# Performance work log

Hardware: AMD Instinct MI355X
Metric: run time of the kernel (lower is better)

Reference implementation:

```python
import jax, jax.numpy as jnp
import numpy as np

B, S, F = 64, 512, 128
H = 512            # LSTM hidden (conv_channels entries)
D0, D1 = 512, 256  # dense_sizes
P, FPP = 24, 4     # predictions, features_per_prediction


def _lstm_layer(x, Wx, Wh, b):
    """Flax OptimizedLSTMCell math: gates i,f,g,o; input matmul has no bias,
    hidden matmul carries the bias; carry initialized to zeros."""
    Bc, Sc, _ = x.shape
    Hc = Wh.shape[0]
    # Precompute input contribution for all timesteps: [B, S, 4H]
    xg = jnp.einsum('bsd,dg->bsg', x, Wx)

    def step(carry, xg_t):
        c, h = carry
        g = xg_t + h @ Wh + b            # [B, 4H]
        i, f, gg, o = jnp.split(g, 4, axis=-1)
        c = jax.nn.sigmoid(f) * c + jax.nn.sigmoid(i) * jnp.tanh(gg)
        h = jax.nn.sigmoid(o) * jnp.tanh(c)
        return (c, h), h

    init = (jnp.zeros((Bc, Hc), x.dtype), jnp.zeros((Bc, Hc), x.dtype))
    _, hs = jax.lax.scan(step, init, jnp.swapaxes(xg, 0, 1))  # [S, B, H]
    return jnp.swapaxes(hs, 0, 1)


def setup_inputs() -> dict:
    key = jax.random.key(0)
    ks = jax.random.split(key, 12)
    g = lambda k, shape, fan_in: jax.random.normal(k, shape, jnp.float32) / np.sqrt(fan_in)
    return {
        'x':    jax.random.normal(ks[0], (B, S, F), jnp.float32),
        'Wx0':  g(ks[1], (F, 4 * H), F),
        'Wh0':  g(ks[2], (H, 4 * H), H),
        'b0':   jnp.zeros((4 * H,), jnp.float32),
        'Wx1':  g(ks[3], (H, 4 * H), H),
        'Wh1':  g(ks[4], (H, 4 * H), H),
        'b1':   jnp.zeros((4 * H,), jnp.float32),
        'Wd0':  g(ks[5], (H, D0), H),
        'bd0':  jnp.zeros((D0,), jnp.float32),
        'Wd1':  g(ks[6], (D0, D1), D0),
        'bd1':  jnp.zeros((D1,), jnp.float32),
        'Wout': g(ks[7], (D1, P * FPP), D1),
        'bout': jnp.zeros((P * FPP,), jnp.float32),
        'train': 0,
    }


def reference(x, Wx0, Wh0, b0, Wx1, Wh1, b1, Wd0, bd0, Wd1, bd1, Wout, bout, train):
    # down_scale == 1 -> no max_pool; dropout == 0 -> no dropout.
    h = _lstm_layer(x, Wx0, Wh0, b0)   # [B, S, H]
    h = _lstm_layer(h, Wx1, Wh1, b1)   # [B, S, H]
    h = h[:, -1, :]                    # last timestep [B, H]
    h = jax.nn.relu(h @ Wd0 + bd0)
    h = jax.nn.relu(h @ Wd1 + bd1)
    out = h @ Wout + bout              # [B, P*FPP]
    out = out.reshape((-1, P, FPP))
    return jax.nn.sigmoid(out)
```

## Files before the change

### kernel.cpp

```cpp
#include <hip/hip_runtime.h>

typedef __attribute__((ext_vector_type(8))) short short8;
typedef __attribute__((ext_vector_type(4))) float f32x4;

#define NB 64
#define NS 512
#define NF 128
#define NH 512
#define NG 2048
#define NBLK 256

__device__ __forceinline__ unsigned short f2bf(float f) {
    unsigned int u = __builtin_bit_cast(unsigned int, f);
    u = (u + 0x7fffu + ((u >> 16) & 1u)) >> 16;
    return (unsigned short)u;
}
__device__ __forceinline__ float sigm(float x) { return 1.0f / (1.0f + __expf(-x)); }
__device__ __forceinline__ float tanh_(float x) {
    float e = __expf(2.0f * fabsf(x));
    float r = 1.0f - 2.0f / (e + 1.0f);
    return x < 0.0f ? -r : r;
}

__device__ __forceinline__ short8 cohld16(const unsigned short* p) {
    unsigned long long* q = (unsigned long long*)p;
    union { unsigned long long u[2]; short8 s; } v;
    v.u[0] = __hip_atomic_load(q,     __ATOMIC_RELAXED, __HIP_MEMORY_SCOPE_AGENT);
    v.u[1] = __hip_atomic_load(q + 1, __ATOMIC_RELAXED, __HIP_MEMORY_SCOPE_AGENT);
    return v.s;
}
__device__ __forceinline__ void cohst2(unsigned short* p, unsigned short v) {
    __hip_atomic_store(p, v, __ATOMIC_RELAXED, __HIP_MEMORY_SCOPE_AGENT);
}

__device__ __forceinline__ void flag_wait(const unsigned* flags, int lane, unsigned tgt) {
    while (__hip_atomic_load(&flags[lane], __ATOMIC_RELAXED, __HIP_MEMORY_SCOPE_AGENT) < tgt)
        __builtin_amdgcn_s_sleep(1);
    __builtin_amdgcn_sched_barrier(0);
    asm volatile("" ::: "memory");
}
__device__ __forceinline__ void flag_signal(unsigned* myflag, unsigned val, int lane) {
    asm volatile("s_waitcnt vmcnt(0)" ::: "memory");
    if (lane == 0)
        __hip_atomic_store(myflag, val, __ATOMIC_RELAXED, __HIP_MEMORY_SCOPE_AGENT);
}

__global__ void cvt_bf16(const float* __restrict__ in, unsigned short* __restrict__ out, int n) {
    int i = blockIdx.x * blockDim.x + threadIdx.x;
    int stride = gridDim.x * blockDim.x;
    for (; i < n; i += stride) out[i] = f2bf(in[i]);
}

__global__ void tr_cvt(const float* __restrict__ in, unsigned short* __restrict__ out, int K, int N) {
    int i = blockIdx.x * blockDim.x + threadIdx.x;
    if (i >= K * N) return;
    int n = i / K, k = i - n * K;
    out[i] = f2bf(in[k * N + n]);
}

__global__ void __launch_bounds__(64, 1) lstm_coop(
    const unsigned short* __restrict__ xbf,
    unsigned short* __restrict__ h0,
    unsigned short* __restrict__ h1,
    const unsigned short* __restrict__ whT0,
    const unsigned short* __restrict__ wxT0,
    const unsigned short* __restrict__ whT1,
    const unsigned short* __restrict__ wxT1,
    const float* __restrict__ b0,
    const float* __restrict__ b1,
    float* __restrict__ hlast,
    unsigned* __restrict__ flagbase)
{
    __shared__ unsigned short w0lds[32 * 640];
    __shared__ unsigned short w1lds[32 * 1024];

    const int lane = threadIdx.x;
    const int c16  = lane & 15;
    const int kg   = lane >> 4;
    const int bg   = blockIdx.x >> 6;
    const int ct   = blockIdx.x & 63;
    unsigned* flagA = (unsigned*)((char*)flagbase + (size_t)bg * 4096);
    unsigned* flagB = (unsigned*)((char*)flagbase + (size_t)bg * 4096 + 2048);

    auto loadw = [&](unsigned short* dst, const unsigned short* whT,
                     const unsigned short* wxT, int Kx, int rowB) {
        int cpr = (NH + Kx) >> 3;
        for (int idx = lane; idx < 32 * cpr; idx += 64) {
            int n = idx / cpr, cc = idx - n * cpr;
            int G = (n >> 3) * NH + ct * 8 + (n & 7);
            uint4 v = (cc < 64) ? *(const uint4*)(whT + (size_t)G * NH + cc * 8)
                                : *(const uint4*)(wxT + (size_t)G * Kx + (size_t)(cc - 64) * 8);
            *(uint4*)((char*)dst + n * rowB + ((cc * 16) ^ ((n & 7) << 4))) = v;
        }
    };
    loadw(w0lds, whT0, wxT0, NF, 1280);
    loadw(w1lds, whT1, wxT1, NH, 2048);
    __syncthreads();

    const int hc8 = c16 & 7;
    const float bi0 = b0[0 * NH + ct * 8 + hc8], bf0 = b0[1 * NH + ct * 8 + hc8];
    const float bg0 = b0[2 * NH + ct * 8 + hc8], bo0 = b0[3 * NH + ct * 8 + hc8];
    const float bi1 = b1[0 * NH + ct * 8 + hc8], bf1 = b1[1 * NH + ct * 8 + hc8];
    const float bg1 = b1[2 * NH + ct * 8 + hc8], bo1 = b1[3 * NH + ct * 8 + hc8];

    const int arow = bg * 16 + c16;
    const size_t aseq = (size_t)arow * NS;
    float cst0[4] = {0.f, 0.f, 0.f, 0.f};
    float cst1[4] = {0.f, 0.f, 0.f, 0.f};

    const char* lA0 = (const char*)w0lds + (size_t)c16 * 1280;
    const char* lB0 = (const char*)w0lds + (size_t)(16 + c16) * 1280;
    const char* lA1 = (const char*)w1lds + (size_t)c16 * 2048;
    const char* lB1 = (const char*)w1lds + (size_t)(16 + c16) * 2048;
    const int swz = (c16 & 7) << 4;

    auto epilogue = [&](f32x4 acc0, f32x4 acc1, float* cst,
                        float bi, float bf_, float bgt, float bo,
                        unsigned short* hseq, int t, bool wlast) {
        f32x4 s0, s1;
        #pragma unroll
        for (int i = 0; i < 4; ++i) {
            s0[i] = __shfl_xor(acc0[i], 8, 64);
            s1[i] = __shfl_xor(acc1[i], 8, 64);
        }
        const bool lower = (c16 < 8);
        unsigned short* hw = hseq + ((size_t)(bg * 16 + kg * 4) * NS + t) * NH + ct * 8 + hc8;
        #pragma unroll
        for (int i = 0; i < 4; ++i) {
            float gi = (lower ? acc0[i] : s0[i]) + bi;
            float gf = (lower ? s0[i] : acc0[i]) + bf_;
            float gg = (lower ? acc1[i] : s1[i]) + bgt;
            float go = (lower ? s1[i] : acc1[i]) + bo;
            float c_ = sigm(gf) * cst[i] + sigm(gi) * tanh_(gg);
            cst[i] = c_;
            float hv = sigm(go) * tanh_(c_);
            if (lower) {
                cohst2(hw + (size_t)i * NS * NH, f2bf(hv));
                if (wlast)
                    hlast[(bg * 16 + kg * 4 + i) * NH + ct * 8 + hc8] = hv;
            }
        }
    };

    short8 hfrag[16];

    for (int r = 0; r <= NS; ++r) {
        if (r > 0) {
            flag_wait(flagA, lane, (unsigned)r);
            const unsigned short* hp = h0 + (aseq + (r - 1)) * NH + kg * 8;
            #pragma unroll
            for (int ks = 0; ks < 16; ++ks) hfrag[ks] = cohld16(hp + ks * 32);
        }
        if (r < NS) {
            f32x4 a0 = {0.f, 0.f, 0.f, 0.f};
            f32x4 a1 = {0.f, 0.f, 0.f, 0.f};
            const unsigned short* xp = xbf + (aseq + r) * NF + kg * 8;
            #pragma unroll
            for (int ks = 0; ks < 4; ++ks) {
                short8 a = *(const short8*)(xp + ks * 32);
                int boff = 1024 + ks * 64 + kg * 16;
                a0 = __builtin_amdgcn_mfma_f32_16x16x32_bf16(a, *(const short8*)(lA0 + (boff ^ swz)), a0, 0, 0, 0);
                a1 = __builtin_amdgcn_mfma_f32_16x16x32_bf16(a, *(const short8*)(lB0 + (boff ^ swz)), a1, 0, 0, 0);
            }
            if (r > 0) {
                #pragma unroll
                for (int ks = 0; ks < 16; ++ks) {
                    int boff = ks * 64 + kg * 16;
                    a0 = __builtin_amdgcn_mfma_f32_16x16x32_bf16(hfrag[ks], *(const short8*)(lA0 + (boff ^ swz)), a0, 0, 0, 0);
                    a1 = __builtin_amdgcn_mfma_f32_16x16x32_bf16(hfrag[ks], *(const short8*)(lB0 + (boff ^ swz)), a1, 0, 0, 0);
                }
            }
            epilogue(a0, a1, cst0, bi0, bf0, bg0, bo0, h0, r, false);
            flag_signal(&flagA[ct], (unsigned)(r + 1), lane);
        }
        if (r > 0) {
            int t1 = r - 1;
            flag_wait(flagB, lane, (unsigned)t1);
            f32x4 a0 = {0.f, 0.f, 0.f, 0.f};
            f32x4 a1 = {0.f, 0.f, 0.f, 0.f};
            #pragma unroll
            for (int ks = 0; ks < 16; ++ks) {
                int boff = 1024 + ks * 64 + kg * 16;
                a0 = __builtin_amdgcn_mfma_f32_16x16x32_bf16(hfrag[ks], *(const short8*)(lA1 + (boff ^ swz)), a0, 0, 0, 0);
                a1 = __builtin_amdgcn_mfma_f32_16x16x32_bf16(hfrag[ks], *(const short8*)(lB1 + (boff ^ swz)), a1, 0, 0, 0);
            }
            if (t1 > 0) {
                const unsigned short* hp = h1 + (aseq + (t1 - 1)) * NH + kg * 8;
                #pragma unroll
                for (int ks = 0; ks < 16; ++ks) {
                    short8 a = cohld16(hp + ks * 32);
                    int boff = ks * 64 + kg * 16;
                    a0 = __builtin_amdgcn_mfma_f32_16x16x32_bf16(a, *(const short8*)(lA1 + (boff ^ swz)), a0, 0, 0, 0);
                    a1 = __builtin_amdgcn_mfma_f32_16x16x32_bf16(a, *(const short8*)(lB1 + (boff ^ swz)), a1, 0, 0, 0);
                }
            }
            epilogue(a0, a1, cst1, bi1, bf1, bg1, bo1, h1, t1, t1 == NS - 1);
            flag_signal(&flagB[ct], (unsigned)(t1 + 1), lane);
        }
    }
}

__global__ void dense(const float* __restrict__ in, const float* __restrict__ W,
                      const float* __restrict__ bias, float* __restrict__ out,
                      int K, int N, int mode) {
    int b = blockIdx.x;
    int j = threadIdx.x;
    extern __shared__ float srow[];
    for (int k = j; k < K; k += blockDim.x) srow[k] = in[b * K + k];
    __syncthreads();
    if (j < N) {
        float acc = bias[j];
        for (int k = 0; k < K; ++k) acc += srow[k] * W[k * N + j];
        if (mode == 1) acc = fmaxf(acc, 0.0f);
        else           acc = 1.0f / (1.0f + __expf(-acc));
        out[b * N + j] = acc;
    }
}

extern "C" void kernel_launch(void* const* d_in, const int* in_sizes, int n_in,
                              void* d_out, int out_size, void* d_ws, size_t ws_size,
                              hipStream_t stream) {
    const float* x    = (const float*)d_in[0];
    const float* Wx0  = (const float*)d_in[1];
    const float* Wh0  = (const float*)d_in[2];
    const float* b0   = (const float*)d_in[3];
    const float* Wx1  = (const float*)d_in[4];
    const float* Wh1  = (const float*)d_in[5];
    const float* b1   = (const float*)d_in[6];
    const float* Wd0  = (const float*)d_in[7];
    const float* bd0  = (const float*)d_in[8];
    const float* Wd1  = (const float*)d_in[9];
    const float* bd1  = (const float*)d_in[10];
    const float* Wout = (const float*)d_in[11];
    const float* bout = (const float*)d_in[12];

    char* ws = (char*)d_ws;
    size_t off = 0;
    auto alloc = [&](size_t bytes) { void* p = ws + off; off += (bytes + 255) & ~255ull; return p; };
    unsigned* flagbase = (unsigned*)alloc(4 * 4096);
    unsigned short* xbf  = (unsigned short*)alloc((size_t)NB * NS * NF * 2);
    unsigned short* h0   = (unsigned short*)alloc((size_t)NB * NS * NH * 2);
    unsigned short* h1   = (unsigned short*)alloc((size_t)NB * NS * NH * 2);
    unsigned short* whT0 = (unsigned short*)alloc((size_t)NG * NH * 2);
    unsigned short* wxT0 = (unsigned short*)alloc((size_t)NG * NF * 2);
    unsigned short* whT1 = (unsigned short*)alloc((size_t)NG * NH * 2);
    unsigned short* wxT1 = (unsigned short*)alloc((size_t)NG * NH * 2);
    float* hlast = (float*)alloc((size_t)NB * NH * 4);
    float* dt0   = (float*)alloc((size_t)NB * 512 * 4);
    float* dt1   = (float*)alloc((size_t)NB * 256 * 4);

    hipMemsetAsync(flagbase, 0, 4 * 4096, stream);
    cvt_bf16<<<2048, 256, 0, stream>>>(x, xbf, NB * NS * NF);
    tr_cvt<<<(NG * NF + 255) / 256, 256, 0, stream>>>(Wx0, wxT0, NF, NG);
    tr_cvt<<<(NG * NH + 255) / 256, 256, 0, stream>>>(Wh0, whT0, NH, NG);
    tr_cvt<<<(NG * NH + 255) / 256, 256, 0, stream>>>(Wx1, wxT1, NH, NG);
    tr_cvt<<<(NG * NH + 255) / 256, 256, 0, stream>>>(Wh1, whT1, NH, NG);

    void* args[] = { (void*)&xbf, (void*)&h0, (void*)&h1,
                     (void*)&whT0, (void*)&wxT0, (void*)&whT1, (void*)&wxT1,
                     (void*)&b0, (void*)&b1, (void*)&hlast, (void*)&flagbase };
    hipLaunchCooperativeKernel((void*)lstm_coop, dim3(NBLK), dim3(64), args, 0, stream);

    dense<<<NB, 512, 512 * 4, stream>>>(hlast, Wd0, bd0, dt0, 512, 512, 1);
    dense<<<NB, 256, 512 * 4, stream>>>(dt0, Wd1, bd1, dt1, 512, 256, 1);
    dense<<<NB, 128, 256 * 4, stream>>>(dt1, Wout, bout, (float*)d_out, 256, 96, 2);
}
```

Before: 4.658 ms.

## Replace flag barriers with tagged double-buffered hidden-state slots polled directly

Drops the per-step flag arrays and stores each hidden value as a 32-bit word that carries a timestep tag in its upper half. Consumers poll the data itself until every tag matches, so the separate flag write, wait and reload round trip goes away. The full h sequences are replaced by two-slot ring buffers, and the layer-0 input matmul now runs before the poll so it overlaps the wait. The cost is twice the bytes per hidden value and a heavier polling loop. Ring-buffer correctness relies on producers never running more than one step ahead of consumers.

```diff
diff --git a/kernel.cpp b/kernel.cpp
--- a/kernel.cpp
+++ b/kernel.cpp
@@ -9,6 +9,7 @@
 #define NH 512
 #define NG 2048
 #define NBLK 256
+#define TH_SLOT (64 * 512)
 
 __device__ __forceinline__ unsigned short f2bf(float f) {
     unsigned int u = __builtin_bit_cast(unsigned int, f);
@@ -22,29 +23,6 @@
     return x < 0.0f ? -r : r;
 }
 
-__device__ __forceinline__ short8 cohld16(const unsigned short* p) {
-    unsigned long long* q = (unsigned long long*)p;
-    union { unsigned long long u[2]; short8 s; } v;
-    v.u[0] = __hip_atomic_load(q,     __ATOMIC_RELAXED, __HIP_MEMORY_SCOPE_AGENT);
-    v.u[1] = __hip_atomic_load(q + 1, __ATOMIC_RELAXED, __HIP_MEMORY_SCOPE_AGENT);
-    return v.s;
-}
-__device__ __forceinline__ void cohst2(unsigned short* p, unsigned short v) {
-    __hip_atomic_store(p, v, __ATOMIC_RELAXED, __HIP_MEMORY_SCOPE_AGENT);
-}
-
-__device__ __forceinline__ void flag_wait(const unsigned* flags, int lane, unsigned tgt) {
-    while (__hip_atomic_load(&flags[lane], __ATOMIC_RELAXED, __HIP_MEMORY_SCOPE_AGENT) < tgt)
-        __builtin_amdgcn_s_sleep(1);
-    __builtin_amdgcn_sched_barrier(0);
-    asm volatile("" ::: "memory");
-}
-__device__ __forceinline__ void flag_signal(unsigned* myflag, unsigned val, int lane) {
-    asm volatile("s_waitcnt vmcnt(0)" ::: "memory");
-    if (lane == 0)
-        __hip_atomic_store(myflag, val, __ATOMIC_RELAXED, __HIP_MEMORY_SCOPE_AGENT);
-}
-
 __global__ void cvt_bf16(const float* __restrict__ in, unsigned short* __restrict__ out, int n) {
     int i = blockIdx.x * blockDim.x + threadIdx.x;
     int stride = gridDim.x * blockDim.x;
@@ -60,16 +38,15 @@
 
 __global__ void __launch_bounds__(64, 1) lstm_coop(
     const unsigned short* __restrict__ xbf,
-    unsigned short* __restrict__ h0,
-    unsigned short* __restrict__ h1,
+    unsigned* __restrict__ th0,
+    unsigned* __restrict__ th1,
     const unsigned short* __restrict__ whT0,
     const unsigned short* __restrict__ wxT0,
     const unsigned short* __restrict__ whT1,
     const unsigned short* __restrict__ wxT1,
     const float* __restrict__ b0,
     const float* __restrict__ b1,
-    float* __restrict__ hlast,
-    unsigned* __restrict__ flagbase)
+    float* __restrict__ hlast)
 {
     __shared__ unsigned short w0lds[32 * 640];
     __shared__ unsigned short w1lds[32 * 1024];
@@ -79,8 +56,6 @@
     const int kg   = lane >> 4;
     const int bg   = blockIdx.x >> 6;
     const int ct   = blockIdx.x & 63;
-    unsigned* flagA = (unsigned*)((char*)flagbase + (size_t)bg * 4096);
-    unsigned* flagB = (unsigned*)((char*)flagbase + (size_t)bg * 4096 + 2048);
 
     auto loadw = [&](unsigned short* dst, const unsigned short* whT,
                      const unsigned short* wxT, int Kx, int rowB) {
@@ -114,9 +89,60 @@
     const char* lB1 = (const char*)w1lds + (size_t)(16 + c16) * 2048;
     const int swz = (c16 & 7) << 4;
 
+    auto poll_tensor = [&](const unsigned* tslot, unsigned want, short8* frag) {
+        const unsigned long long* p0 =
+            (const unsigned long long*)(tslot + (size_t)arow * NH) + kg * 4;
+        for (int b = 0; b < 2; ++b) {
+            for (;;) {
+                unsigned bad = 0;
+                #pragma unroll
+                for (int j = 0; j < 8; ++j) {
+                    unsigned w0 = __hip_atomic_load(
+                        (const unsigned*)(p0 + (size_t)(b * 8 + j) * 16),
+                        __ATOMIC_RELAXED, __HIP_MEMORY_SCOPE_AGENT);
+                    bad |= (w0 >> 16) ^ want;
+                }
+                if (__ballot(bad != 0) == 0ull) break;
+            }
+            for (;;) {
+                unsigned long long d[8][4];
+                #pragma unroll
+                for (int j = 0; j < 8; ++j)
+                    #pragma unroll
+                    for (int w = 0; w < 4; ++w)
+                        d[j][w] = __hip_atomic_load(
+                            p0 + (size_t)(b * 8 + j) * 16 + w,
+                            __ATOMIC_RELAXED, __HIP_MEMORY_SCOPE_AGENT);
+                unsigned bad = 0;
+                #pragma unroll
+                for (int j = 0; j < 8; ++j)
+                    #pragma unroll
+                    for (int w = 0; w < 4; ++w) {
+                        unsigned long long x = d[j][w];
+                        bad |= (((unsigned)(x >> 16) & 0xFFFFu) ^ want)
+                             | ((unsigned)(x >> 48) ^ want);
+                    }
+                if (__ballot(bad != 0) == 0ull) {
+                    #pragma unroll
+                    for (int j = 0; j < 8; ++j) {
+                        short8 s;
+                        #pragma unroll
+                        for (int w = 0; w < 4; ++w) {
+                            s[2 * w]     = (short)(unsigned short)(d[j][w] & 0xFFFFu);
+                            s[2 * w + 1] = (short)(unsigned short)((d[j][w] >> 32) & 0xFFFFu);
+                        }
+                        frag[b * 8 + j] = s;
+                    }
+                    break;
+                }
+            }
+        }
+        __builtin_amdgcn_sched_barrier(0);
+    };
+
     auto epilogue = [&](f32x4 acc0, f32x4 acc1, float* cst,
                         float bi, float bf_, float bgt, float bo,
-                        unsigned short* hseq, int t, bool wlast) {
+                        unsigned* tslot, unsigned tag, bool wlast) {
         f32x4 s0, s1;
         #pragma unroll
         for (int i = 0; i < 4; ++i) {
@@ -124,7 +150,7 @@
             s1[i] = __shfl_xor(acc1[i], 8, 64);
         }
         const bool lower = (c16 < 8);
-        unsigned short* hw = hseq + ((size_t)(bg * 16 + kg * 4) * NS + t) * NH + ct * 8 + hc8;
+        unsigned* tw = tslot + (size_t)(bg * 16 + kg * 4) * NH + ct * 8 + hc8;
         #pragma unroll
         for (int i = 0; i < 4; ++i) {
             float gi = (lower ? acc0[i] : s0[i]) + bi;
@@ -135,7 +161,9 @@
             cst[i] = c_;
             float hv = sigm(go) * tanh_(c_);
             if (lower) {
-                cohst2(hw + (size_t)i * NS * NH, f2bf(hv));
+                __hip_atomic_store(tw + (size_t)i * NH,
+                                   (tag << 16) | (unsigned)f2bf(hv),
+                                   __ATOMIC_RELAXED, __HIP_MEMORY_SCOPE_AGENT);
                 if (wlast)
                     hlast[(bg * 16 + kg * 4 + i) * NH + ct * 8 + hc8] = hv;
             }
@@ -145,15 +173,9 @@
     short8 hfrag[16];
 
     for (int r = 0; r <= NS; ++r) {
-        if (r > 0) {
-            flag_wait(flagA, lane, (unsigned)r);
-            const unsigned short* hp = h0 + (aseq + (r - 1)) * NH + kg * 8;
-            #pragma unroll
-            for (int ks = 0; ks < 16; ++ks) hfrag[ks] = cohld16(hp + ks * 32);
-        }
+        f32x4 a0 = {0.f, 0.f, 0.f, 0.f};
+        f32x4 a1 = {0.f, 0.f, 0.f, 0.f};
         if (r < NS) {
-            f32x4 a0 = {0.f, 0.f, 0.f, 0.f};
-            f32x4 a1 = {0.f, 0.f, 0.f, 0.f};
             const unsigned short* xp = xbf + (aseq + r) * NF + kg * 8;
             #pragma unroll
             for (int ks = 0; ks < 4; ++ks) {
@@ -162,6 +184,9 @@
                 a0 = __builtin_amdgcn_mfma_f32_16x16x32_bf16(a, *(const short8*)(lA0 + (boff ^ swz)), a0, 0, 0, 0);
                 a1 = __builtin_amdgcn_mfma_f32_16x16x32_bf16(a, *(const short8*)(lB0 + (boff ^ swz)), a1, 0, 0, 0);
             }
+        }
+        if (r > 0) poll_tensor(th0 + ((r - 1) & 1) * TH_SLOT, (unsigned)r, hfrag);
+        if (r < NS) {
             if (r > 0) {
                 #pragma unroll
                 for (int ks = 0; ks < 16; ++ks) {
@@ -170,32 +195,30 @@
                     a1 = __builtin_amdgcn_mfma_f32_16x16x32_bf16(hfrag[ks], *(const short8*)(lB0 + (boff ^ swz)), a1, 0, 0, 0);
                 }
             }
-            epilogue(a0, a1, cst0, bi0, bf0, bg0, bo0, h0, r, false);
-            flag_signal(&flagA[ct], (unsigned)(r + 1), lane);
+            epilogue(a0, a1, cst0, bi0, bf0, bg0, bo0,
+                     th0 + (r & 1) * TH_SLOT, (unsigned)(r + 1), false);
         }
         if (r > 0) {
             int t1 = r - 1;
-            flag_wait(flagB, lane, (unsigned)t1);
-            f32x4 a0 = {0.f, 0.f, 0.f, 0.f};
-            f32x4 a1 = {0.f, 0.f, 0.f, 0.f};
+            f32x4 c0 = {0.f, 0.f, 0.f, 0.f};
+            f32x4 c1 = {0.f, 0.f, 0.f, 0.f};
             #pragma unroll
             for (int ks = 0; ks < 16; ++ks) {
                 int boff = 1024 + ks * 64 + kg * 16;
-                a0 = __builtin_amdgcn_mfma_f32_16x16x32_bf16(hfrag[ks], *(const short8*)(lA1 + (boff ^ swz)), a0, 0, 0, 0);
-                a1 = __builtin_amdgcn_mfma_f32_16x16x32_bf16(hfrag[ks], *(const short8*)(lB1 + (boff ^ swz)), a1, 0, 0, 0);
+                c0 = __builtin_amdgcn_mfma_f32_16x16x32_bf16(hfrag[ks], *(const short8*)(lA1 + (boff ^ swz)), c0, 0, 0, 0);
+                c1 = __builtin_amdgcn_mfma_f32_16x16x32_bf16(hfrag[ks], *(const short8*)(lB1 + (boff ^ swz)), c1, 0, 0, 0);
             }
             if (t1 > 0) {
-                const unsigned short* hp = h1 + (aseq + (t1 - 1)) * NH + kg * 8;
+                poll_tensor(th1 + (r & 1) * TH_SLOT, (unsigned)t1, hfrag);
                 #pragma unroll
                 for (int ks = 0; ks < 16; ++ks) {
-                    short8 a = cohld16(hp + ks * 32);
                     int boff = ks * 64 + kg * 16;
-                    a0 = __builtin_amdgcn_mfma_f32_16x16x32_bf16(a, *(const short8*)(lA1 + (boff ^ swz)), a0, 0, 0, 0);
-                    a1 = __builtin_amdgcn_mfma_f32_16x16x32_bf16(a, *(const short8*)(lB1 + (boff ^ swz)), a1, 0, 0, 0);
-                }
-            }
-            epilogue(a0, a1, cst1, bi1, bf1, bg1, bo1, h1, t1, t1 == NS - 1);
-            flag_signal(&flagB[ct], (unsigned)(t1 + 1), lane);
+                    c0 = __builtin_amdgcn_mfma_f32_16x16x32_bf16(hfrag[ks], *(const short8*)(lA1 + (boff ^ swz)), c0, 0, 0, 0);
+                    c1 = __builtin_amdgcn_mfma_f32_16x16x32_bf16(hfrag[ks], *(const short8*)(lB1 + (boff ^ swz)), c1, 0, 0, 0);
+                }
+            }
+            epilogue(c0, c1, cst1, bi1, bf1, bg1, bo1,
+                     th1 + (t1 & 1) * TH_SLOT, (unsigned)(t1 + 1), t1 == NS - 1);
         }
     }
 }
@@ -237,10 +260,9 @@
     char* ws = (char*)d_ws;
     size_t off = 0;
     auto alloc = [&](size_t bytes) { void* p = ws + off; off += (bytes + 255) & ~255ull; return p; };
-    unsigned* flagbase = (unsigned*)alloc(4 * 4096);
+    unsigned* th0 = (unsigned*)alloc((size_t)2 * TH_SLOT * 4);
+    unsigned* th1 = (unsigned*)alloc((size_t)2 * TH_SLOT * 4);
     unsigned short* xbf  = (unsigned short*)alloc((size_t)NB * NS * NF * 2);
-    unsigned short* h0   = (unsigned short*)alloc((size_t)NB * NS * NH * 2);
-    unsigned short* h1   = (unsigned short*)alloc((size_t)NB * NS * NH * 2);
     unsigned short* whT0 = (unsigned short*)alloc((size_t)NG * NH * 2);
     unsigned short* wxT0 = (unsigned short*)alloc((size_t)NG * NF * 2);
     unsigned short* whT1 = (unsigned short*)alloc((size_t)NG * NH * 2);
@@ -249,16 +271,16 @@
     float* dt0   = (float*)alloc((size_t)NB * 512 * 4);
     float* dt1   = (float*)alloc((size_t)NB * 256 * 4);
 
-    hipMemsetAsync(flagbase, 0, 4 * 4096, stream);
+    hipMemsetAsync(th0, 0, (size_t)4 * TH_SLOT * 4, stream);
     cvt_bf16<<<2048, 256, 0, stream>>>(x, xbf, NB * NS * NF);
     tr_cvt<<<(NG * NF + 255) / 256, 256, 0, stream>>>(Wx0, wxT0, NF, NG);
     tr_cvt<<<(NG * NH + 255) / 256, 256, 0, stream>>>(Wh0, whT0, NH, NG);
     tr_cvt<<<(NG * NH + 255) / 256, 256, 0, stream>>>(Wx1, wxT1, NH, NG);
     tr_cvt<<<(NG * NH + 255) / 256, 256, 0, stream>>>(Wh1, whT1, NH, NG);
 
-    void* args[] = { (void*)&xbf, (void*)&h0, (void*)&h1,
+    void* args[] = { (void*)&xbf, (void*)&th0, (void*)&th1,
                      (void*)&whT0, (void*)&wxT0, (void*)&whT1, (void*)&wxT1,
-                     (void*)&b0, (void*)&b1, (void*)&hlast, (void*)&flagbase };
+                     (void*)&b0, (void*)&b1, (void*)&hlast };
     hipLaunchCooperativeKernel((void*)lstm_coop, dim3(NBLK), dim3(64), args, 0, stream);
 
     dense<<<NB, 512, 512 * 4, stream>>>(hlast, Wd0, bd0, dt0, 512, 512, 1);
```

Result: slower. 6.023 ms (+29.3%).
